# Kernel tuning notes

Hardware: AMD Instinct MI355X
Metric: run time of the kernel (lower is better)

Reference implementation:

```python
import jax, jax.numpy as jnp
import numpy as np

DIM = 1024
NUM_HEADS = 16
HEAD_DIM = DIM // NUM_HEADS
ROPE_BASE = 10000.0


def _rope_cache(seq_len, head_dim, dtype=jnp.float32):
    inv_freq = 1.0 / (ROPE_BASE ** (jnp.arange(0, head_dim, 2, dtype=jnp.float32) / head_dim))
    t = jnp.arange(seq_len, dtype=jnp.float32)
    freqs = jnp.einsum('i,j->ij', t, inv_freq)          # [S, hd/2]
    emb = jnp.concatenate([freqs, freqs], axis=-1)       # [S, hd]
    return jnp.cos(emb).astype(dtype), jnp.sin(emb).astype(dtype)


def _rotate_half(x):
    x1, x2 = jnp.split(x, 2, axis=-1)
    return jnp.concatenate([-x2, x1], axis=-1)


def setup_inputs() -> dict:
    key = jax.random.key(0)
    k1, k2, k3 = jax.random.split(key, 3)
    B, S, D = 2, 2048, DIM
    x = jax.random.normal(k1, (B, S, D), dtype=jnp.float32)
    mask = jnp.tril(jnp.ones((S, S), dtype=jnp.bool_))   # causal mask
    w_qkv = jax.random.normal(k2, (D, 3 * D), dtype=jnp.float32) * (D ** -0.5)
    w_out = jax.random.normal(k3, (D, D), dtype=jnp.float32) * (D ** -0.5)
    return {"x": x, "w_qkv": w_qkv, "w_out": w_out, "mask": mask}


def reference(x, w_qkv, w_out, mask):
    B, S, D = x.shape
    H, hd = NUM_HEADS, HEAD_DIM
    qkv = x @ w_qkv                                       # [B,S,3D]
    q, k, v = jnp.split(qkv, 3, axis=-1)
    # [B,H,S,hd]
    q = q.reshape(B, S, H, hd).transpose(0, 2, 1, 3)
    k = k.reshape(B, S, H, hd).transpose(0, 2, 1, 3)
    v = v.reshape(B, S, H, hd).transpose(0, 2, 1, 3)
    cos, sin = _rope_cache(S, hd, q.dtype)               # [S,hd]
    q = q * cos + _rotate_half(q) * sin
    k = k * cos + _rotate_half(k) * sin
    scale = hd ** -0.5
    scores = jnp.einsum('bhqd,bhkd->bhqk', q, k) * scale  # [B,H,S,S]
    neg = jnp.finfo(scores.dtype).min
    scores = jnp.where(mask[None, None, :, :], scores, neg)
    attn = jax.nn.softmax(scores, axis=-1)                # dropout off (eval)
    out = jnp.einsum('bhqk,bhkd->bhqd', attn, v)
    out = out.transpose(0, 2, 1, 3).reshape(B, S, D)
    return out @ w_out
```

## Files before the change

### kernel.cpp

```cpp
#include <hip/hip_runtime.h>

typedef __attribute__((ext_vector_type(8))) short short8;
typedef __attribute__((ext_vector_type(4))) float f32x4;
typedef __attribute__((ext_vector_type(16))) float f32x16;

__device__ __forceinline__ unsigned short f2bf(float f) {
    unsigned u = __builtin_bit_cast(unsigned, f);
    u += 0x7FFFu + ((u >> 16) & 1u);
    return (unsigned short)(u >> 16);
}
__device__ __forceinline__ short8 ld_frag(const uint4* p, size_t idx16) {
    return __builtin_bit_cast(short8, p[idx16]);
}
__device__ __forceinline__ unsigned cvt_pk_bf16(float lo, float hi) {
    unsigned r;
    asm("v_cvt_pk_bf16_f32 %0, %1, %2" : "=v"(r) : "v"(lo), "v"(hi));
    return r;
}
__device__ __forceinline__ void gload_lds16(const void* g, void* l) {
    __builtin_amdgcn_global_load_lds((const __attribute__((address_space(1))) void*)g,
                                     (__attribute__((address_space(3))) void*)l, 16, 0, 0);
}

__global__ __launch_bounds__(256) void prep_kernel(const float* __restrict__ x, unsigned short* __restrict__ xb,
                                                   const float* __restrict__ wqkv, unsigned short* __restrict__ wqkvT,
                                                   const float* __restrict__ wout, unsigned short* __restrict__ woutT,
                                                   float* __restrict__ cosT, float* __restrict__ sinT) {
    __shared__ float t[32][33];
    int bid = blockIdx.x, tid = threadIdx.x;
    if (bid < 256) {
        int idx = bid * 256 + tid;
        int s = idx >> 5, i = idx & 31;
        float inv = powf(10000.f, -(float)i / 32.f);
        float ang = (float)s * inv;
        cosT[idx] = cosf(ang);
        sinT[idx] = sinf(ang);
        return;
    }
    if (bid < 4352) {
        int i = (bid - 256) * 256 + tid;
        float4 v = reinterpret_cast<const float4*>(x)[i];
        ushort4 o;
        o.x = f2bf(v.x); o.y = f2bf(v.y); o.z = f2bf(v.z); o.w = f2bf(v.w);
        reinterpret_cast<ushort4*>(xb)[i] = o;
        return;
    }
    const float* in; unsigned short* out; int R, C, c0, r0;
    if (bid < 7424) {
        int b2 = bid - 4352;
        in = wqkv; out = wqkvT; R = 1024; C = 3072;
        c0 = (b2 % 96) * 32; r0 = (b2 / 96) * 32;
    } else {
        int b2 = bid - 7424;
        in = wout; out = woutT; R = 1024; C = 1024;
        c0 = (b2 % 32) * 32; r0 = (b2 / 32) * 32;
    }
    int tx = tid & 31, ty = tid >> 5;
    for (int i = 0; i < 4; ++i)
        t[ty + i * 8][tx] = in[(size_t)(r0 + ty + i * 8) * C + c0 + tx];
    __syncthreads();
    for (int i = 0; i < 4; ++i)
        out[(size_t)(c0 + ty + i * 8) * R + r0 + tx] = f2bf(t[tx][ty + i * 8]);
}

template <bool OUT_BF16, int NF>
__global__ __launch_bounds__(256) void gemm_bt_kernel(const unsigned short* __restrict__ A,
                                                      const unsigned short* __restrict__ Bt,
                                                      void* __restrict__ Cout,
                                                      int M, int N, int K) {
    constexpr int BN = NF * 32;
    __shared__ __align__(16) unsigned short As[2][128 * 32];
    __shared__ __align__(16) unsigned short Bs[2][BN * 32];
    int tid = threadIdx.x;
    int lane = tid & 63;
    int w = tid >> 6;
    int wm = w >> 1, wn = w & 1;
    int m0 = blockIdx.y * 128, n0 = blockIdx.x * BN;
    int rq = lane >> 4, cl = lane & 15;

    f32x4 acc[4][NF] = {};
    const uint4* As4 = reinterpret_cast<const uint4*>(As);
    const uint4* Bs4 = reinterpret_cast<const uint4*>(Bs);

    #pragma unroll
    for (int i = 0; i < 2; ++i) {
        int c = i * 256 + tid;
        int r = c >> 2, cc = c & 3;
        gload_lds16(A + (size_t)(m0 + r) * K + cc * 8,
                    (char*)As[0] + (size_t)(i * 256 + w * 64) * 16);
    }
    #pragma unroll
    for (int i = 0; i < NF / 2; ++i) {
        int c = i * 256 + tid;
        int r = c >> 2, cc = c & 3;
        gload_lds16(Bt + (size_t)(n0 + r) * K + cc * 8,
                    (char*)Bs[0] + (size_t)(i * 256 + w * 64) * 16);
    }
    __syncthreads();
    int cur = 0;

    for (int k0 = 0; k0 < K; k0 += 32) {
        short8 af[4], bfr[NF];
        #pragma unroll
        for (int mf = 0; mf < 4; ++mf) {
            int row = wm * 64 + mf * 16 + cl;
            af[mf] = ld_frag(As4, cur * 512 + row * 4 + rq);
        }
        #pragma unroll
        for (int nf = 0; nf < NF; ++nf) {
            int row = wn * (NF * 16) + nf * 16 + cl;
            bfr[nf] = ld_frag(Bs4, cur * (NF * 128) + row * 4 + rq);
        }
        if (k0 + 32 < K) {
            int kn = k0 + 32;
            #pragma unroll
            for (int i = 0; i < 2; ++i) {
                int c = i * 256 + tid;
                int r = c >> 2, cc = c & 3;
                gload_lds16(A + (size_t)(m0 + r) * K + kn + cc * 8,
                            (char*)As[cur ^ 1] + (size_t)(i * 256 + w * 64) * 16);
            }
            #pragma unroll
            for (int i = 0; i < NF / 2; ++i) {
                int c = i * 256 + tid;
                int r = c >> 2, cc = c & 3;
                gload_lds16(Bt + (size_t)(n0 + r) * K + kn + cc * 8,
                            (char*)Bs[cur ^ 1] + (size_t)(i * 256 + w * 64) * 16);
            }
        }
        __builtin_amdgcn_s_setprio(1);
        #pragma unroll
        for (int mf = 0; mf < 4; ++mf)
            #pragma unroll
            for (int nf = 0; nf < NF; ++nf)
                acc[mf][nf] = __builtin_amdgcn_mfma_f32_16x16x32_bf16(af[mf], bfr[nf], acc[mf][nf], 0, 0, 0);
        __builtin_amdgcn_s_setprio(0);
        __syncthreads();
        cur ^= 1;
    }
    #pragma unroll
    for (int mf = 0; mf < 4; ++mf)
        #pragma unroll
        for (int nf = 0; nf < NF; ++nf)
            #pragma unroll
            for (int r = 0; r < 4; ++r) {
                size_t row = m0 + wm * 64 + mf * 16 + rq * 4 + r;
                size_t col = n0 + wn * (NF * 16) + nf * 16 + cl;
                float v = acc[mf][nf][r];
                if (OUT_BF16)
                    ((unsigned short*)Cout)[row * N + col] = f2bf(v);
                else
                    ((float*)Cout)[row * N + col] = v;
            }
}

__global__ __launch_bounds__(256) void gemm_qkv_rope_kernel(const unsigned short* __restrict__ A,
                                                            const unsigned short* __restrict__ Bt,
                                                            const float* __restrict__ cosT,
                                                            const float* __restrict__ sinT,
                                                            unsigned short* __restrict__ Qb,
                                                            unsigned short* __restrict__ Kb,
                                                            unsigned short* __restrict__ VT) {
    const int K = 1024;
    __shared__ __align__(16) unsigned short As[2][128 * 32];
    __shared__ __align__(16) unsigned short Bs[2][128 * 32];
    int tid = threadIdx.x;
    int lane = tid & 63;
    int w = tid >> 6;
    int wm = w >> 1, wn = w & 1;
    int m0 = blockIdx.y * 128, n0 = blockIdx.x * 128;
    int rq = lane >> 4, cl = lane & 15;

    f32x4 acc[4][4] = {};
    const uint4* As4 = reinterpret_cast<const uint4*>(As);
    const uint4* Bs4 = reinterpret_cast<const uint4*>(Bs);

    #pragma unroll
    for (int i = 0; i < 2; ++i) {
        int c = i * 256 + tid;
        int r = c >> 2, cc = c & 3;
        gload_lds16(A + (size_t)(m0 + r) * K + cc * 8,
                    (char*)As[0] + (size_t)(i * 256 + w * 64) * 16);
        gload_lds16(Bt + (size_t)(n0 + r) * K + cc * 8,
                    (char*)Bs[0] + (size_t)(i * 256 + w * 64) * 16);
    }
    __syncthreads();
    int cur = 0;

    for (int k0 = 0; k0 < K; k0 += 32) {
        short8 af[4], bfr[4];
        #pragma unroll
        for (int mf = 0; mf < 4; ++mf)
            af[mf] = ld_frag(As4, cur * 512 + (wm * 64 + mf * 16 + cl) * 4 + rq);
        #pragma unroll
        for (int nf = 0; nf < 4; ++nf)
            bfr[nf] = ld_frag(Bs4, cur * 512 + (wn * 64 + nf * 16 + cl) * 4 + rq);
        if (k0 + 32 < K) {
            int kn = k0 + 32;
            #pragma unroll
            for (int i = 0; i < 2; ++i) {
                int c = i * 256 + tid;
                int r = c >> 2, cc = c & 3;
                gload_lds16(A + (size_t)(m0 + r) * K + kn + cc * 8,
                            (char*)As[cur ^ 1] + (size_t)(i * 256 + w * 64) * 16);
                gload_lds16(Bt + (size_t)(n0 + r) * K + kn + cc * 8,
                            (char*)Bs[cur ^ 1] + (size_t)(i * 256 + w * 64) * 16);
            }
        }
        __builtin_amdgcn_s_setprio(1);
        #pragma unroll
        for (int mf = 0; mf < 4; ++mf)
            #pragma unroll
            for (int nf = 0; nf < 4; ++nf)
                acc[mf][nf] = __builtin_amdgcn_mfma_f32_16x16x32_bf16(af[mf], bfr[nf], acc[mf][nf], 0, 0, 0);
        __builtin_amdgcn_s_setprio(0);
        __syncthreads();
        cur ^= 1;
    }

    const float QSCALE = 0.125f * 1.44269504088896f;
    int colbase = n0 + wn * 64;
    int sect = colbase >> 10;
    int h = (colbase >> 6) & 15;
    #pragma unroll
    for (int mf = 0; mf < 4; ++mf) {
        int row0 = m0 + wm * 64 + mf * 16 + rq * 4;
        int b = row0 >> 11;
        int s0r = row0 & 2047;
        size_t ho = (size_t)(b * 16 + h);
        if (sect == 2) {
            #pragma unroll
            for (int nf = 0; nf < 4; ++nf) {
                int d = nf * 16 + cl;
                ushort4 o;
                o.x = f2bf(acc[mf][nf][0]);
                o.y = f2bf(acc[mf][nf][1]);
                o.z = f2bf(acc[mf][nf][2]);
                o.w = f2bf(acc[mf][nf][3]);
                *reinterpret_cast<ushort4*>(VT + (ho * 64 + d) * 2048 + s0r) = o;
            }
        } else {
            unsigned short* dst = (sect == 0) ? Qb : Kb;
            float scale = (sect == 0) ? QSCALE : 1.0f;
            #pragma unroll
            for (int nf = 0; nf < 4; ++nf) {
                int d = nf * 16 + cl;
                int f = ((nf & 1) << 4) + cl;
                #pragma unroll
                for (int r = 0; r < 4; ++r) {
                    int s = s0r + r;
                    float cs = cosT[s * 32 + f], sn = sinT[s * 32 + f];
                    float val = acc[mf][nf][r], pair = acc[mf][nf ^ 2][r];
                    float out = (nf < 2) ? val * cs - pair * sn : val * cs + pair * sn;
                    dst[(ho * 2048 + s) * 64 + d] = f2bf(out * scale);
                }
            }
        }
    }
}

__global__ __launch_bounds__(256) void flash_attn_kernel(const unsigned short* __restrict__ Qb,
                                                         const unsigned short* __restrict__ Kb,
                                                         const unsigned short* __restrict__ VT,
                                                         unsigned short* __restrict__ Oattn) {
    const int S = 2048;
    __shared__ __align__(16) char smem[4 * 8192 + 512];
    char* KsB = smem;
    char* VsB = smem + 2 * 8192;
    int tid = threadIdx.x, lane = tid & 63, w = tid >> 6;
    int qsub = w & 1, kvh = w >> 1;
    int gid = blockIdx.x;
    int hh = gid & 31;
    int cp = gid >> 5;
    size_t headOff = (size_t)hh * S * 64;
    const unsigned short* Kg = Kb + headOff;
    const unsigned short* Vg = VT + headOff;
    const uint4* Qg4 = reinterpret_cast<const uint4*>(Qb + headOff);
    int l31 = lane & 31, hi = lane >> 5;

    int sr[2], sj[2];
    #pragma unroll
    for (int i = 0; i < 2; ++i) {
        int cch = i * 256 + tid;
        sr[i] = cch >> 3;
        sj[i] = ((cch & 7) ^ (sr[i] & 7)) * 8;
    }
    float* mo = reinterpret_cast<float*>(smem);
    float* ml = reinterpret_cast<float*>(smem + 16384);

    #pragma unroll
    for (int ph = 0; ph < 2; ++ph) {
        int c = ph ? (31 - cp) : cp;
        int q0 = c * 64;
        int qw = q0 + qsub * 32;
        int qrow = qw + l31;

        short8 qf[4];
        #pragma unroll
        for (int cc = 0; cc < 4; ++cc)
            qf[cc] = ld_frag(Qg4, (size_t)qrow * 8 + cc * 2 + hi);

        f32x16 oacc0 = {}, oacc1 = {};
        float l = 0.f;
        int nk = c + 1;

        #pragma unroll
        for (int i = 0; i < 2; ++i) {
            gload_lds16(Kg + sr[i] * 64 + sj[i], KsB + (i * 256 + w * 64) * 16);
            gload_lds16(Vg + (size_t)sr[i] * S + sj[i], VsB + (i * 256 + w * 64) * 16);
        }
        __syncthreads();
        int cur = 0;

        for (int kt = 0; kt < nk; ++kt) {
            int kv0 = kt * 64;
            int kvbase = kv0 + kvh * 32;
            bool active = kvbase <= qw + 31;
            short8 ka[4], va[4];
            if (active) {
                const char* Kt = KsB + cur * 8192;
                const char* Vt = VsB + cur * 8192;
                int r = kvh * 32 + l31;
                #pragma unroll
                for (int cc = 0; cc < 4; ++cc)
                    ka[cc] = __builtin_bit_cast(short8, *reinterpret_cast<const uint4*>(
                        Kt + r * 128 + (((2 * cc + hi) ^ (r & 7)) * 16)));
                #pragma unroll
                for (int t = 0; t < 2; ++t) {
                    va[t] = __builtin_bit_cast(short8, *reinterpret_cast<const uint4*>(
                        Vt + l31 * 128 + (((kvh * 4 + 2 * t + hi) ^ (l31 & 7)) * 16)));
                    va[2 + t] = __builtin_bit_cast(short8, *reinterpret_cast<const uint4*>(
                        Vt + (32 + l31) * 128 + (((kvh * 4 + 2 * t + hi) ^ ((32 + l31) & 7)) * 16)));
                }
            }
            if (kt + 1 < nk) {
                int kn = kv0 + 64;
                #pragma unroll
                for (int i = 0; i < 2; ++i) {
                    gload_lds16(Kg + (kn + sr[i]) * 64 + sj[i],
                                KsB + (cur ^ 1) * 8192 + (i * 256 + w * 64) * 16);
                    gload_lds16(Vg + (size_t)sr[i] * S + kn + sj[i],
                                VsB + (cur ^ 1) * 8192 + (i * 256 + w * 64) * 16);
                }
            }
            if (active) {
                f32x16 s = {};
                __builtin_amdgcn_s_setprio(1);
                #pragma unroll
                for (int cc = 0; cc < 4; ++cc)
                    s = __builtin_amdgcn_mfma_f32_32x32x16_bf16(ka[cc], qf[cc], s, 0, 0, 0);
                __builtin_amdgcn_s_setprio(0);

                if (kvbase + 31 > qw) {
                    #pragma unroll
                    for (int r = 0; r < 16; ++r) {
                        int kva = kvbase + (r & 3) + 8 * (r >> 2) + 4 * hi;
                        s[r] = (kva <= qrow) ? s[r] : -1e30f;
                    }
                }
                #pragma unroll
                for (int r = 0; r < 16; ++r) s[r] = exp2f(s[r]);
                float rp0 = ((s[0] + s[4]) + (s[8] + s[12])) + ((s[1] + s[5]) + (s[9] + s[13]));
                float rp1 = ((s[2] + s[6]) + (s[10] + s[14])) + ((s[3] + s[7]) + (s[11] + s[15]));
                float rs = rp0 + rp1;
                rs += __shfl_xor(rs, 32);
                l += rs;

                unsigned wd[8];
                #pragma unroll
                for (int i = 0; i < 8; ++i) wd[i] = cvt_pk_bf16(s[2 * i], s[2 * i + 1]);
                unsigned e0 = (unsigned)__shfl_xor((int)(hi ? wd[0] : wd[2]), 32);
                unsigned e1 = (unsigned)__shfl_xor((int)(hi ? wd[1] : wd[3]), 32);
                unsigned e2 = (unsigned)__shfl_xor((int)(hi ? wd[4] : wd[6]), 32);
                unsigned e3 = (unsigned)__shfl_xor((int)(hi ? wd[5] : wd[7]), 32);
                uint4 p0 = hi ? uint4{e0, e1, wd[2], wd[3]} : uint4{wd[0], wd[1], e0, e1};
                uint4 p1 = hi ? uint4{e2, e3, wd[6], wd[7]} : uint4{wd[4], wd[5], e2, e3};
                short8 pb0 = __builtin_bit_cast(short8, p0);
                short8 pb1 = __builtin_bit_cast(short8, p1);

                __builtin_amdgcn_s_setprio(1);
                oacc0 = __builtin_amdgcn_mfma_f32_32x32x16_bf16(va[0], pb0, oacc0, 0, 0, 0);
                oacc0 = __builtin_amdgcn_mfma_f32_32x32x16_bf16(va[1], pb1, oacc0, 0, 0, 0);
                oacc1 = __builtin_amdgcn_mfma_f32_32x32x16_bf16(va[2], pb0, oacc1, 0, 0, 0);
                oacc1 = __builtin_amdgcn_mfma_f32_32x32x16_bf16(va[3], pb1, oacc1, 0, 0, 0);
                __builtin_amdgcn_s_setprio(0);
            }
            __syncthreads();
            cur ^= 1;
        }

        if (kvh) {
            #pragma unroll
            for (int r = 0; r < 16; ++r) {
                mo[(r * 2 + qsub) * 64 + lane]        = oacc0[r];
                mo[((16 + r) * 2 + qsub) * 64 + lane] = oacc1[r];
            }
            ml[qsub * 64 + lane] = l;
        }
        __syncthreads();
        if (!kvh) {
            l += ml[qsub * 64 + lane];
            float invl = 1.f / l;
            size_t orow = ((size_t)((hh >> 4) * 2048 + qrow)) * 1024 + (hh & 15) * 64;
            #pragma unroll
            for (int du = 0; du < 2; ++du) {
                const f32x16& oa = du ? oacc1 : oacc0;
                #pragma unroll
                for (int gq = 0; gq < 4; ++gq) {
                    ushort4 o;
                    #pragma unroll
                    for (int e = 0; e < 4; ++e) {
                        int r = 4 * gq + e;
                        float v = (oa[r] + mo[((du * 16 + r) * 2 + qsub) * 64 + lane]) * invl;
                        ((unsigned short*)&o)[e] = f2bf(v);
                    }
                    int d = du * 32 + 4 * hi + 8 * gq;
                    *reinterpret_cast<ushort4*>(Oattn + orow + d) = o;
                }
            }
        }
        __syncthreads();
    }
}

extern "C" void kernel_launch(void* const* d_in, const int* in_sizes, int n_in,
                              void* d_out, int out_size, void* d_ws, size_t ws_size,
                              hipStream_t stream) {
    const float* x    = (const float*)d_in[0];
    const float* wqkv = (const float*)d_in[1];
    const float* wout = (const float*)d_in[2];

    char* ws = (char*)d_ws;
    unsigned short* xb    = (unsigned short*)(ws);
    unsigned short* wqkvT = (unsigned short*)(ws + (8ull  << 20));
    unsigned short* woutT = (unsigned short*)(ws + (14ull << 20));
    unsigned short* Qb    = (unsigned short*)(ws + (40ull << 20));
    unsigned short* Kb    = (unsigned short*)(ws + (48ull << 20));
    unsigned short* VT    = (unsigned short*)(ws + (56ull << 20));
    unsigned short* Oat   = (unsigned short*)(ws + (64ull << 20));
    float* cosT           = (float*)(ws + (72ull << 20));
    float* sinT           = (float*)(ws + (72ull << 20) + (256u << 10));

    prep_kernel<<<8448, 256, 0, stream>>>(x, xb, wqkv, wqkvT, wout, woutT, cosT, sinT);
    gemm_qkv_rope_kernel<<<dim3(24, 32), 256, 0, stream>>>(xb, wqkvT, cosT, sinT, Qb, Kb, VT);
    flash_attn_kernel<<<512, 256, 0, stream>>>(Qb, Kb, VT, Oat);
    gemm_bt_kernel<false, 2><<<dim3(16, 32), 256, 0, stream>>>(Oat, woutT, d_out, 4096, 1024, 1024);
}
```

Baseline: 113.5 us.

## Triple-buffer LDS staging with explicit vmcnt waits in GEMMs and attention

Moves the two GEMM kernels and the attention kernel from double-buffered LDS staging to a three-stage ring. Prefetch now runs two tiles ahead, and each iteration waits with a partial s_waitcnt vmcnt and one barrier instead of a full __syncthreads at the end. The aim is to hide more global-load latency and cut the barrier cost per K step. In exchange it uses more LDS per block, which may lower occupancy, and it depends on the hand-tuned vmcnt counts matching the number of loads each thread issues.

```diff
diff --git a/kernel.cpp b/kernel.cpp
--- a/kernel.cpp
+++ b/kernel.cpp
@@ -21,6 +21,9 @@
     __builtin_amdgcn_global_load_lds((const __attribute__((address_space(1))) void*)g,
                                      (__attribute__((address_space(3))) void*)l, 16, 0, 0);
 }
+__device__ __forceinline__ void wait_vm4() { asm volatile("s_waitcnt vmcnt(4)" ::: "memory"); __builtin_amdgcn_sched_barrier(0); }
+__device__ __forceinline__ void wait_vm3() { asm volatile("s_waitcnt vmcnt(3)" ::: "memory"); __builtin_amdgcn_sched_barrier(0); }
+__device__ __forceinline__ void wait_vm0() { asm volatile("s_waitcnt vmcnt(0)" ::: "memory"); __builtin_amdgcn_sched_barrier(0); }
 
 __global__ __launch_bounds__(256) void prep_kernel(const float* __restrict__ x, unsigned short* __restrict__ xb,
                                                    const float* __restrict__ wqkv, unsigned short* __restrict__ wqkvT,
@@ -69,8 +72,8 @@
                                                       void* __restrict__ Cout,
                                                       int M, int N, int K) {
     constexpr int BN = NF * 32;
-    __shared__ __align__(16) unsigned short As[2][128 * 32];
-    __shared__ __align__(16) unsigned short Bs[2][BN * 32];
+    __shared__ __align__(16) unsigned short As[3][128 * 32];
+    __shared__ __align__(16) unsigned short Bs[3][BN * 32];
     int tid = threadIdx.x;
     int lane = tid & 63;
     int w = tid >> 6;
@@ -82,51 +85,44 @@
     const uint4* As4 = reinterpret_cast<const uint4*>(As);
     const uint4* Bs4 = reinterpret_cast<const uint4*>(Bs);
 
-    #pragma unroll
-    for (int i = 0; i < 2; ++i) {
-        int c = i * 256 + tid;
-        int r = c >> 2, cc = c & 3;
-        gload_lds16(A + (size_t)(m0 + r) * K + cc * 8,
-                    (char*)As[0] + (size_t)(i * 256 + w * 64) * 16);
-    }
-    #pragma unroll
-    for (int i = 0; i < NF / 2; ++i) {
-        int c = i * 256 + tid;
-        int r = c >> 2, cc = c & 3;
-        gload_lds16(Bt + (size_t)(n0 + r) * K + cc * 8,
-                    (char*)Bs[0] + (size_t)(i * 256 + w * 64) * 16);
-    }
-    __syncthreads();
-    int cur = 0;
-
-    for (int k0 = 0; k0 < K; k0 += 32) {
+    auto stage = [&](int k0, int buf) {
+        #pragma unroll
+        for (int i = 0; i < 2; ++i) {
+            int c = i * 256 + tid;
+            int r = c >> 2, cc = c & 3;
+            gload_lds16(A + (size_t)(m0 + r) * K + k0 + cc * 8,
+                        (char*)As[buf] + (size_t)(i * 256 + w * 64) * 16);
+        }
+        #pragma unroll
+        for (int i = 0; i < NF / 2; ++i) {
+            int c = i * 256 + tid;
+            int r = c >> 2, cc = c & 3;
+            gload_lds16(Bt + (size_t)(n0 + r) * K + k0 + cc * 8,
+                        (char*)Bs[buf] + (size_t)(i * 256 + w * 64) * 16);
+        }
+    };
+
+    int nk = K / 32;
+    stage(0, 0);
+    if (nk > 1) stage(32, 1);
+    int b0 = 0, b2 = 2;
+
+    for (int it = 0; it < nk; ++it) {
+        if (it + 1 < nk) { if constexpr (NF == 2) wait_vm3(); else wait_vm4(); }
+        else             wait_vm0();
+        __builtin_amdgcn_s_barrier();
+        if (it + 2 < nk) stage((it + 2) * 32, b2);
+
         short8 af[4], bfr[NF];
         #pragma unroll
         for (int mf = 0; mf < 4; ++mf) {
             int row = wm * 64 + mf * 16 + cl;
-            af[mf] = ld_frag(As4, cur * 512 + row * 4 + rq);
+            af[mf] = ld_frag(As4, b0 * 512 + row * 4 + rq);
         }
         #pragma unroll
         for (int nf = 0; nf < NF; ++nf) {
             int row = wn * (NF * 16) + nf * 16 + cl;
-            bfr[nf] = ld_frag(Bs4, cur * (NF * 128) + row * 4 + rq);
-        }
-        if (k0 + 32 < K) {
-            int kn = k0 + 32;
-            #pragma unroll
-            for (int i = 0; i < 2; ++i) {
-                int c = i * 256 + tid;
-                int r = c >> 2, cc = c & 3;
-                gload_lds16(A + (size_t)(m0 + r) * K + kn + cc * 8,
-                            (char*)As[cur ^ 1] + (size_t)(i * 256 + w * 64) * 16);
-            }
-            #pragma unroll
-            for (int i = 0; i < NF / 2; ++i) {
-                int c = i * 256 + tid;
-                int r = c >> 2, cc = c & 3;
-                gload_lds16(Bt + (size_t)(n0 + r) * K + kn + cc * 8,
-                            (char*)Bs[cur ^ 1] + (size_t)(i * 256 + w * 64) * 16);
-            }
+            bfr[nf] = ld_frag(Bs4, b0 * (NF * 128) + row * 4 + rq);
         }
         __builtin_amdgcn_s_setprio(1);
         #pragma unroll
@@ -135,8 +131,8 @@
             for (int nf = 0; nf < NF; ++nf)
                 acc[mf][nf] = __builtin_amdgcn_mfma_f32_16x16x32_bf16(af[mf], bfr[nf], acc[mf][nf], 0, 0, 0);
         __builtin_amdgcn_s_setprio(0);
-        __syncthreads();
-        cur ^= 1;
+        b0 = (b0 == 2) ? 0 : b0 + 1;
+        b2 = (b2 == 2) ? 0 : b2 + 1;
     }
     #pragma unroll
     for (int mf = 0; mf < 4; ++mf)
@@ -162,8 +158,8 @@
                                                             unsigned short* __restrict__ Kb,
                                                             unsigned short* __restrict__ VT) {
     const int K = 1024;
-    __shared__ __align__(16) unsigned short As[2][128 * 32];
-    __shared__ __align__(16) unsigned short Bs[2][128 * 32];
+    __shared__ __align__(16) unsigned short As[3][128 * 32];
+    __shared__ __align__(16) unsigned short Bs[3][128 * 32];
     int tid = threadIdx.x;
     int lane = tid & 63;
     int w = tid >> 6;
@@ -175,38 +171,35 @@
     const uint4* As4 = reinterpret_cast<const uint4*>(As);
     const uint4* Bs4 = reinterpret_cast<const uint4*>(Bs);
 
-    #pragma unroll
-    for (int i = 0; i < 2; ++i) {
-        int c = i * 256 + tid;
-        int r = c >> 2, cc = c & 3;
-        gload_lds16(A + (size_t)(m0 + r) * K + cc * 8,
-                    (char*)As[0] + (size_t)(i * 256 + w * 64) * 16);
-        gload_lds16(Bt + (size_t)(n0 + r) * K + cc * 8,
-                    (char*)Bs[0] + (size_t)(i * 256 + w * 64) * 16);
-    }
-    __syncthreads();
-    int cur = 0;
-
-    for (int k0 = 0; k0 < K; k0 += 32) {
+    auto stage = [&](int k0, int buf) {
+        #pragma unroll
+        for (int i = 0; i < 2; ++i) {
+            int c = i * 256 + tid;
+            int r = c >> 2, cc = c & 3;
+            gload_lds16(A + (size_t)(m0 + r) * K + k0 + cc * 8,
+                        (char*)As[buf] + (size_t)(i * 256 + w * 64) * 16);
+            gload_lds16(Bt + (size_t)(n0 + r) * K + k0 + cc * 8,
+                        (char*)Bs[buf] + (size_t)(i * 256 + w * 64) * 16);
+        }
+    };
+
+    stage(0, 0);
+    stage(32, 1);
+    int b0 = 0, b2 = 2;
+
+    for (int it = 0; it < 32; ++it) {
+        if (it + 1 < 32) wait_vm4();
+        else             wait_vm0();
+        __builtin_amdgcn_s_barrier();
+        if (it + 2 < 32) stage((it + 2) * 32, b2);
+
         short8 af[4], bfr[4];
         #pragma unroll
         for (int mf = 0; mf < 4; ++mf)
-            af[mf] = ld_frag(As4, cur * 512 + (wm * 64 + mf * 16 + cl) * 4 + rq);
+            af[mf] = ld_frag(As4, b0 * 512 + (wm * 64 + mf * 16 + cl) * 4 + rq);
         #pragma unroll
         for (int nf = 0; nf < 4; ++nf)
-            bfr[nf] = ld_frag(Bs4, cur * 512 + (wn * 64 + nf * 16 + cl) * 4 + rq);
-        if (k0 + 32 < K) {
-            int kn = k0 + 32;
-            #pragma unroll
-            for (int i = 0; i < 2; ++i) {
-                int c = i * 256 + tid;
-                int r = c >> 2, cc = c & 3;
-                gload_lds16(A + (size_t)(m0 + r) * K + kn + cc * 8,
-                            (char*)As[cur ^ 1] + (size_t)(i * 256 + w * 64) * 16);
-                gload_lds16(Bt + (size_t)(n0 + r) * K + kn + cc * 8,
-                            (char*)Bs[cur ^ 1] + (size_t)(i * 256 + w * 64) * 16);
-            }
-        }
+            bfr[nf] = ld_frag(Bs4, b0 * 512 + (wn * 64 + nf * 16 + cl) * 4 + rq);
         __builtin_amdgcn_s_setprio(1);
         #pragma unroll
         for (int mf = 0; mf < 4; ++mf)
@@ -214,8 +207,8 @@
             for (int nf = 0; nf < 4; ++nf)
                 acc[mf][nf] = __builtin_amdgcn_mfma_f32_16x16x32_bf16(af[mf], bfr[nf], acc[mf][nf], 0, 0, 0);
         __builtin_amdgcn_s_setprio(0);
-        __syncthreads();
-        cur ^= 1;
+        b0 = (b0 == 2) ? 0 : b0 + 1;
+        b2 = (b2 == 2) ? 0 : b2 + 1;
     }
 
     const float QSCALE = 0.125f * 1.44269504088896f;
@@ -264,9 +257,7 @@
                                                          const unsigned short* __restrict__ VT,
                                                          unsigned short* __restrict__ Oattn) {
     const int S = 2048;
-    __shared__ __align__(16) char smem[4 * 8192 + 512];
-    char* KsB = smem;
-    char* VsB = smem + 2 * 8192;
+    __shared__ __align__(16) char smem[3 * 16384 + 512];
     int tid = threadIdx.x, lane = tid & 63, w = tid >> 6;
     int qsub = w & 1, kvh = w >> 1;
     int gid = blockIdx.x;
@@ -286,7 +277,17 @@
         sj[i] = ((cch & 7) ^ (sr[i] & 7)) * 8;
     }
     float* mo = reinterpret_cast<float*>(smem);
-    float* ml = reinterpret_cast<float*>(smem + 16384);
+    float* ml = reinterpret_cast<float*>(smem + 3 * 16384);
+
+    auto stage = [&](int kt, int b) {
+        char* base = smem + b * 16384;
+        int kn = kt * 64;
+        #pragma unroll
+        for (int i = 0; i < 2; ++i) {
+            gload_lds16(Kg + (size_t)(kn + sr[i]) * 64 + sj[i], base + (i * 256 + w * 64) * 16);
+            gload_lds16(Vg + (size_t)sr[i] * S + kn + sj[i], base + 8192 + (i * 256 + w * 64) * 16);
+        }
+    };
 
     #pragma unroll
     for (int ph = 0; ph < 2; ++ph) {
@@ -304,22 +305,21 @@
         float l = 0.f;
         int nk = c + 1;
 
-        #pragma unroll
-        for (int i = 0; i < 2; ++i) {
-            gload_lds16(Kg + sr[i] * 64 + sj[i], KsB + (i * 256 + w * 64) * 16);
-            gload_lds16(Vg + (size_t)sr[i] * S + sj[i], VsB + (i * 256 + w * 64) * 16);
-        }
-        __syncthreads();
-        int cur = 0;
+        stage(0, 0);
+        if (nk > 1) stage(1, 1);
+        int b0 = 0, b2 = 2;
 
         for (int kt = 0; kt < nk; ++kt) {
-            int kv0 = kt * 64;
-            int kvbase = kv0 + kvh * 32;
-            bool active = kvbase <= qw + 31;
-            short8 ka[4], va[4];
-            if (active) {
-                const char* Kt = KsB + cur * 8192;
-                const char* Vt = VsB + cur * 8192;
+            if (kt + 1 < nk) wait_vm4();
+            else             wait_vm0();
+            __builtin_amdgcn_s_barrier();
+            if (kt + 2 < nk) stage(kt + 2, b2);
+
+            int kvbase = kt * 64 + kvh * 32;
+            if (kvbase <= qw + 31) {
+                const char* Kt = smem + b0 * 16384;
+                const char* Vt = Kt + 8192;
+                short8 ka[4], va[4];
                 int r = kvh * 32 + l31;
                 #pragma unroll
                 for (int cc = 0; cc < 4; ++cc)
@@ -332,18 +332,7 @@
                     va[2 + t] = __builtin_bit_cast(short8, *reinterpret_cast<const uint4*>(
                         Vt + (32 + l31) * 128 + (((kvh * 4 + 2 * t + hi) ^ ((32 + l31) & 7)) * 16)));
                 }
-            }
-            if (kt + 1 < nk) {
-                int kn = kv0 + 64;
-                #pragma unroll
-                for (int i = 0; i < 2; ++i) {
-                    gload_lds16(Kg + (kn + sr[i]) * 64 + sj[i],
-                                KsB + (cur ^ 1) * 8192 + (i * 256 + w * 64) * 16);
-                    gload_lds16(Vg + (size_t)sr[i] * S + kn + sj[i],
-                                VsB + (cur ^ 1) * 8192 + (i * 256 + w * 64) * 16);
-                }
-            }
-            if (active) {
+
                 f32x16 s = {};
                 __builtin_amdgcn_s_setprio(1);
                 #pragma unroll
@@ -353,13 +342,13 @@
 
                 if (kvbase + 31 > qw) {
                     #pragma unroll
-                    for (int r = 0; r < 16; ++r) {
-                        int kva = kvbase + (r & 3) + 8 * (r >> 2) + 4 * hi;
-                        s[r] = (kva <= qrow) ? s[r] : -1e30f;
+                    for (int r2 = 0; r2 < 16; ++r2) {
+                        int kva = kvbase + (r2 & 3) + 8 * (r2 >> 2) + 4 * hi;
+                        s[r2] = (kva <= qrow) ? s[r2] : -1e30f;
                     }
                 }
                 #pragma unroll
-                for (int r = 0; r < 16; ++r) s[r] = exp2f(s[r]);
+                for (int r2 = 0; r2 < 16; ++r2) s[r2] = exp2f(s[r2]);
                 float rp0 = ((s[0] + s[4]) + (s[8] + s[12])) + ((s[1] + s[5]) + (s[9] + s[13]));
                 float rp1 = ((s[2] + s[6]) + (s[10] + s[14])) + ((s[3] + s[7]) + (s[11] + s[15]));
                 float rs = rp0 + rp1;
@@ -385,9 +374,11 @@
                 oacc1 = __builtin_amdgcn_mfma_f32_32x32x16_bf16(va[3], pb1, oacc1, 0, 0, 0);
                 __builtin_amdgcn_s_setprio(0);
             }
-            __syncthreads();
-            cur ^= 1;
-        }
+            b0 = (b0 == 2) ? 0 : b0 + 1;
+            b2 = (b2 == 2) ? 0 : b2 + 1;
+        }
+
+        __syncthreads();
 
         if (kvh) {
             #pragma unroll
```

After: 118.1 us. 1.04x slower.

## Process both paired causal query chunks concurrently in one KV sweep

Applied to the files above, without the earlier changes.

The flash attention kernel used to handle its two paired query chunks (cp and 31-cp) one after the other, streaming the K/V tiles twice. Now wave pairs split the two chunks and each wave covers 64 query rows against its 32-key slice. All chunks share a single sweep of 32-cp K/V tiles, so each tile is loaded once for both chunks and the per-phase prologue and syncs go away. The cost is doubled accumulator registers (four f32x16), which may reduce occupancy, and waves on the short chunk idle for most rounds.

```diff
diff --git a/kernel.cpp b/kernel.cpp
--- a/kernel.cpp
+++ b/kernel.cpp
@@ -264,11 +264,9 @@
                                                          const unsigned short* __restrict__ VT,
                                                          unsigned short* __restrict__ Oattn) {
     const int S = 2048;
-    __shared__ __align__(16) char smem[4 * 8192 + 512];
-    char* KsB = smem;
-    char* VsB = smem + 2 * 8192;
+    __shared__ __align__(16) char smem[2 * 16384 + 1024];
     int tid = threadIdx.x, lane = tid & 63, w = tid >> 6;
-    int qsub = w & 1, kvh = w >> 1;
+    int half = w & 1, kvh = w >> 1;
     int gid = blockIdx.x;
     int hh = gid & 31;
     int cp = gid >> 5;
@@ -278,6 +276,11 @@
     const uint4* Qg4 = reinterpret_cast<const uint4*>(Qb + headOff);
     int l31 = lane & 31, hi = lane >> 5;
 
+    int c = half ? (31 - cp) : cp;
+    int q0 = c * 64;
+    int nk = c + 1;
+    int rounds = 32 - cp;
+
     int sr[2], sj[2];
     #pragma unroll
     for (int i = 0; i < 2; ++i) {
@@ -285,86 +288,78 @@
         sr[i] = cch >> 3;
         sj[i] = ((cch & 7) ^ (sr[i] & 7)) * 8;
     }
-    float* mo = reinterpret_cast<float*>(smem);
-    float* ml = reinterpret_cast<float*>(smem + 16384);
-
-    #pragma unroll
-    for (int ph = 0; ph < 2; ++ph) {
-        int c = ph ? (31 - cp) : cp;
-        int q0 = c * 64;
-        int qw = q0 + qsub * 32;
-        int qrow = qw + l31;
-
-        short8 qf[4];
+
+    short8 qf[2][4];
+    #pragma unroll
+    for (int qh = 0; qh < 2; ++qh)
         #pragma unroll
         for (int cc = 0; cc < 4; ++cc)
-            qf[cc] = ld_frag(Qg4, (size_t)qrow * 8 + cc * 2 + hi);
-
-        f32x16 oacc0 = {}, oacc1 = {};
-        float l = 0.f;
-        int nk = c + 1;
-
+            qf[qh][cc] = ld_frag(Qg4, (size_t)(q0 + qh * 32 + l31) * 8 + cc * 2 + hi);
+
+    f32x16 oacc00 = {}, oacc01 = {}, oacc10 = {}, oacc11 = {};
+    float l0 = 0.f, l1 = 0.f;
+
+    auto stage = [&](int kt, int b) {
+        char* base = smem + b * 16384;
+        int kn = kt * 64;
         #pragma unroll
         for (int i = 0; i < 2; ++i) {
-            gload_lds16(Kg + sr[i] * 64 + sj[i], KsB + (i * 256 + w * 64) * 16);
-            gload_lds16(Vg + (size_t)sr[i] * S + sj[i], VsB + (i * 256 + w * 64) * 16);
-        }
-        __syncthreads();
-        int cur = 0;
-
-        for (int kt = 0; kt < nk; ++kt) {
-            int kv0 = kt * 64;
-            int kvbase = kv0 + kvh * 32;
-            bool active = kvbase <= qw + 31;
-            short8 ka[4], va[4];
-            if (active) {
-                const char* Kt = KsB + cur * 8192;
-                const char* Vt = VsB + cur * 8192;
-                int r = kvh * 32 + l31;
-                #pragma unroll
-                for (int cc = 0; cc < 4; ++cc)
-                    ka[cc] = __builtin_bit_cast(short8, *reinterpret_cast<const uint4*>(
-                        Kt + r * 128 + (((2 * cc + hi) ^ (r & 7)) * 16)));
-                #pragma unroll
-                for (int t = 0; t < 2; ++t) {
-                    va[t] = __builtin_bit_cast(short8, *reinterpret_cast<const uint4*>(
-                        Vt + l31 * 128 + (((kvh * 4 + 2 * t + hi) ^ (l31 & 7)) * 16)));
-                    va[2 + t] = __builtin_bit_cast(short8, *reinterpret_cast<const uint4*>(
-                        Vt + (32 + l31) * 128 + (((kvh * 4 + 2 * t + hi) ^ ((32 + l31) & 7)) * 16)));
-                }
-            }
-            if (kt + 1 < nk) {
-                int kn = kv0 + 64;
-                #pragma unroll
-                for (int i = 0; i < 2; ++i) {
-                    gload_lds16(Kg + (kn + sr[i]) * 64 + sj[i],
-                                KsB + (cur ^ 1) * 8192 + (i * 256 + w * 64) * 16);
-                    gload_lds16(Vg + (size_t)sr[i] * S + kn + sj[i],
-                                VsB + (cur ^ 1) * 8192 + (i * 256 + w * 64) * 16);
-                }
-            }
-            if (active) {
+            gload_lds16(Kg + (size_t)(kn + sr[i]) * 64 + sj[i], base + (i * 256 + w * 64) * 16);
+            gload_lds16(Vg + (size_t)sr[i] * S + kn + sj[i], base + 8192 + (i * 256 + w * 64) * 16);
+        }
+    };
+
+    stage(0, 0);
+    __syncthreads();
+    int cur = 0;
+
+    for (int kt = 0; kt < rounds; ++kt) {
+        bool active = kt < nk;
+        int kvbase = kt * 64 + kvh * 32;
+        short8 ka[4], va[4];
+        if (active) {
+            const char* Kt = smem + cur * 16384;
+            const char* Vt = Kt + 8192;
+            int r = kvh * 32 + l31;
+            #pragma unroll
+            for (int cc = 0; cc < 4; ++cc)
+                ka[cc] = __builtin_bit_cast(short8, *reinterpret_cast<const uint4*>(
+                    Kt + r * 128 + (((2 * cc + hi) ^ (r & 7)) * 16)));
+            #pragma unroll
+            for (int t = 0; t < 2; ++t) {
+                va[t] = __builtin_bit_cast(short8, *reinterpret_cast<const uint4*>(
+                    Vt + l31 * 128 + (((kvh * 4 + 2 * t + hi) ^ (l31 & 7)) * 16)));
+                va[2 + t] = __builtin_bit_cast(short8, *reinterpret_cast<const uint4*>(
+                    Vt + (32 + l31) * 128 + (((kvh * 4 + 2 * t + hi) ^ ((32 + l31) & 7)) * 16)));
+            }
+        }
+        if (kt + 1 < rounds) stage(kt + 1, cur ^ 1);
+        if (active) {
+            #pragma unroll
+            for (int qh = 0; qh < 2; ++qh) {
+                int qwq = q0 + qh * 32;
+                int qrow = qwq + l31;
                 f32x16 s = {};
                 __builtin_amdgcn_s_setprio(1);
                 #pragma unroll
                 for (int cc = 0; cc < 4; ++cc)
-                    s = __builtin_amdgcn_mfma_f32_32x32x16_bf16(ka[cc], qf[cc], s, 0, 0, 0);
+                    s = __builtin_amdgcn_mfma_f32_32x32x16_bf16(ka[cc], qh ? qf[1][cc] : qf[0][cc], s, 0, 0, 0);
                 __builtin_amdgcn_s_setprio(0);
 
-                if (kvbase + 31 > qw) {
+                if (kvbase + 31 > qwq) {
                     #pragma unroll
-                    for (int r = 0; r < 16; ++r) {
-                        int kva = kvbase + (r & 3) + 8 * (r >> 2) + 4 * hi;
-                        s[r] = (kva <= qrow) ? s[r] : -1e30f;
+                    for (int r2 = 0; r2 < 16; ++r2) {
+                        int kva = kvbase + (r2 & 3) + 8 * (r2 >> 2) + 4 * hi;
+                        s[r2] = (kva <= qrow) ? s[r2] : -1e30f;
                     }
                 }
                 #pragma unroll
-                for (int r = 0; r < 16; ++r) s[r] = exp2f(s[r]);
+                for (int r2 = 0; r2 < 16; ++r2) s[r2] = exp2f(s[r2]);
                 float rp0 = ((s[0] + s[4]) + (s[8] + s[12])) + ((s[1] + s[5]) + (s[9] + s[13]));
                 float rp1 = ((s[2] + s[6]) + (s[10] + s[14])) + ((s[3] + s[7]) + (s[11] + s[15]));
                 float rs = rp0 + rp1;
                 rs += __shfl_xor(rs, 32);
-                l += rs;
+                if (qh) l1 += rs; else l0 += rs;
 
                 unsigned wd[8];
                 #pragma unroll
@@ -379,39 +374,55 @@
                 short8 pb1 = __builtin_bit_cast(short8, p1);
 
                 __builtin_amdgcn_s_setprio(1);
-                oacc0 = __builtin_amdgcn_mfma_f32_32x32x16_bf16(va[0], pb0, oacc0, 0, 0, 0);
-                oacc0 = __builtin_amdgcn_mfma_f32_32x32x16_bf16(va[1], pb1, oacc0, 0, 0, 0);
-                oacc1 = __builtin_amdgcn_mfma_f32_32x32x16_bf16(va[2], pb0, oacc1, 0, 0, 0);
-                oacc1 = __builtin_amdgcn_mfma_f32_32x32x16_bf16(va[3], pb1, oacc1, 0, 0, 0);
+                if (qh) {
+                    oacc10 = __builtin_amdgcn_mfma_f32_32x32x16_bf16(va[0], pb0, oacc10, 0, 0, 0);
+                    oacc10 = __builtin_amdgcn_mfma_f32_32x32x16_bf16(va[1], pb1, oacc10, 0, 0, 0);
+                    oacc11 = __builtin_amdgcn_mfma_f32_32x32x16_bf16(va[2], pb0, oacc11, 0, 0, 0);
+                    oacc11 = __builtin_amdgcn_mfma_f32_32x32x16_bf16(va[3], pb1, oacc11, 0, 0, 0);
+                } else {
+                    oacc00 = __builtin_amdgcn_mfma_f32_32x32x16_bf16(va[0], pb0, oacc00, 0, 0, 0);
+                    oacc00 = __builtin_amdgcn_mfma_f32_32x32x16_bf16(va[1], pb1, oacc00, 0, 0, 0);
+                    oacc01 = __builtin_amdgcn_mfma_f32_32x32x16_bf16(va[2], pb0, oacc01, 0, 0, 0);
+                    oacc01 = __builtin_amdgcn_mfma_f32_32x32x16_bf16(va[3], pb1, oacc01, 0, 0, 0);
+                }
                 __builtin_amdgcn_s_setprio(0);
             }
-            __syncthreads();
-            cur ^= 1;
-        }
-
-        if (kvh) {
-            #pragma unroll
-            for (int r = 0; r < 16; ++r) {
-                mo[(r * 2 + qsub) * 64 + lane]        = oacc0[r];
-                mo[((16 + r) * 2 + qsub) * 64 + lane] = oacc1[r];
-            }
-            ml[qsub * 64 + lane] = l;
         }
         __syncthreads();
-        if (!kvh) {
-            l += ml[qsub * 64 + lane];
+        cur ^= 1;
+    }
+
+    float* mo = reinterpret_cast<float*>(smem);
+    float* ml = reinterpret_cast<float*>(smem + 32768);
+    if (kvh) {
+        #pragma unroll
+        for (int r = 0; r < 16; ++r) {
+            mo[((half * 2 + 0) * 32 + r) * 64 + lane]      = oacc00[r];
+            mo[((half * 2 + 0) * 32 + 16 + r) * 64 + lane] = oacc01[r];
+            mo[((half * 2 + 1) * 32 + r) * 64 + lane]      = oacc10[r];
+            mo[((half * 2 + 1) * 32 + 16 + r) * 64 + lane] = oacc11[r];
+        }
+        ml[(half * 2 + 0) * 64 + lane] = l0;
+        ml[(half * 2 + 1) * 64 + lane] = l1;
+    }
+    __syncthreads();
+    if (!kvh) {
+        #pragma unroll
+        for (int qh = 0; qh < 2; ++qh) {
+            float l = (qh ? l1 : l0) + ml[(half * 2 + qh) * 64 + lane];
             float invl = 1.f / l;
+            int qrow = q0 + qh * 32 + l31;
             size_t orow = ((size_t)((hh >> 4) * 2048 + qrow)) * 1024 + (hh & 15) * 64;
             #pragma unroll
             for (int du = 0; du < 2; ++du) {
-                const f32x16& oa = du ? oacc1 : oacc0;
+                const f32x16& oa = qh ? (du ? oacc11 : oacc10) : (du ? oacc01 : oacc00);
                 #pragma unroll
                 for (int gq = 0; gq < 4; ++gq) {
                     ushort4 o;
                     #pragma unroll
                     for (int e = 0; e < 4; ++e) {
                         int r = 4 * gq + e;
-                        float v = (oa[r] + mo[((du * 16 + r) * 2 + qsub) * 64 + lane]) * invl;
+                        float v = (oa[r] + mo[((half * 2 + qh) * 32 + du * 16 + r) * 64 + lane]) * invl;
                         ((unsigned short*)&o)[e] = f2bf(v);
                     }
                     int d = du * 32 + 4 * hi + 8 * gq;
@@ -419,7 +430,6 @@
                 }
             }
         }
-        __syncthreads();
     }
 }
 
```

Measured after the change: 156.2 us. 37.6% more time.

## Stage two KV tiles per round to halve barrier count in flash attention

Applied to the files above, without the earlier changes.

The flash attention loop now loads two 64-row K/V tiles per pipeline stage into a larger double-buffered shared memory region (64KB). It processes both tiles before a single __syncthreads, so the main loop takes half as many barriers and prefetches twice as much data ahead. In exchange the block uses more LDS, which may lower occupancy, and the prefetch of round rd+1 is issued after the first sub-tile's fragment loads.

```diff
diff --git a/kernel.cpp b/kernel.cpp
--- a/kernel.cpp
+++ b/kernel.cpp
@@ -264,9 +264,7 @@
                                                          const unsigned short* __restrict__ VT,
                                                          unsigned short* __restrict__ Oattn) {
     const int S = 2048;
-    __shared__ __align__(16) char smem[4 * 8192 + 512];
-    char* KsB = smem;
-    char* VsB = smem + 2 * 8192;
+    __shared__ __align__(16) char smem[2 * 32768 + 512];
     int tid = threadIdx.x, lane = tid & 63, w = tid >> 6;
     int qsub = w & 1, kvh = w >> 1;
     int gid = blockIdx.x;
@@ -303,87 +301,100 @@
         f32x16 oacc0 = {}, oacc1 = {};
         float l = 0.f;
         int nk = c + 1;
-
-        #pragma unroll
-        for (int i = 0; i < 2; ++i) {
-            gload_lds16(Kg + sr[i] * 64 + sj[i], KsB + (i * 256 + w * 64) * 16);
-            gload_lds16(Vg + (size_t)sr[i] * S + sj[i], VsB + (i * 256 + w * 64) * 16);
-        }
+        int nr = (nk + 1) >> 1;
+
+        auto stage2 = [&](int rd, int b) {
+            char* base = smem + b * 32768;
+            #pragma unroll
+            for (int sub = 0; sub < 2; ++sub) {
+                int kt = 2 * rd + sub;
+                if (kt < nk) {
+                    int kn = kt * 64;
+                    #pragma unroll
+                    for (int i = 0; i < 2; ++i) {
+                        gload_lds16(Kg + (size_t)(kn + sr[i]) * 64 + sj[i],
+                                    base + sub * 8192 + (i * 256 + w * 64) * 16);
+                        gload_lds16(Vg + (size_t)sr[i] * S + kn + sj[i],
+                                    base + 16384 + sub * 8192 + (i * 256 + w * 64) * 16);
+                    }
+                }
+            }
+        };
+
+        stage2(0, 0);
         __syncthreads();
         int cur = 0;
 
-        for (int kt = 0; kt < nk; ++kt) {
-            int kv0 = kt * 64;
-            int kvbase = kv0 + kvh * 32;
-            bool active = kvbase <= qw + 31;
-            short8 ka[4], va[4];
-            if (active) {
-                const char* Kt = KsB + cur * 8192;
-                const char* Vt = VsB + cur * 8192;
-                int r = kvh * 32 + l31;
-                #pragma unroll
-                for (int cc = 0; cc < 4; ++cc)
-                    ka[cc] = __builtin_bit_cast(short8, *reinterpret_cast<const uint4*>(
-                        Kt + r * 128 + (((2 * cc + hi) ^ (r & 7)) * 16)));
-                #pragma unroll
-                for (int t = 0; t < 2; ++t) {
-                    va[t] = __builtin_bit_cast(short8, *reinterpret_cast<const uint4*>(
-                        Vt + l31 * 128 + (((kvh * 4 + 2 * t + hi) ^ (l31 & 7)) * 16)));
-                    va[2 + t] = __builtin_bit_cast(short8, *reinterpret_cast<const uint4*>(
-                        Vt + (32 + l31) * 128 + (((kvh * 4 + 2 * t + hi) ^ ((32 + l31) & 7)) * 16)));
-                }
-            }
-            if (kt + 1 < nk) {
-                int kn = kv0 + 64;
-                #pragma unroll
-                for (int i = 0; i < 2; ++i) {
-                    gload_lds16(Kg + (kn + sr[i]) * 64 + sj[i],
-                                KsB + (cur ^ 1) * 8192 + (i * 256 + w * 64) * 16);
-                    gload_lds16(Vg + (size_t)sr[i] * S + kn + sj[i],
-                                VsB + (cur ^ 1) * 8192 + (i * 256 + w * 64) * 16);
-                }
-            }
-            if (active) {
-                f32x16 s = {};
-                __builtin_amdgcn_s_setprio(1);
-                #pragma unroll
-                for (int cc = 0; cc < 4; ++cc)
-                    s = __builtin_amdgcn_mfma_f32_32x32x16_bf16(ka[cc], qf[cc], s, 0, 0, 0);
-                __builtin_amdgcn_s_setprio(0);
-
-                if (kvbase + 31 > qw) {
-                    #pragma unroll
-                    for (int r = 0; r < 16; ++r) {
-                        int kva = kvbase + (r & 3) + 8 * (r >> 2) + 4 * hi;
-                        s[r] = (kva <= qrow) ? s[r] : -1e30f;
+        for (int rd = 0; rd < nr; ++rd) {
+            bool staged = false;
+            #pragma unroll
+            for (int sub = 0; sub < 2; ++sub) {
+                int kt = 2 * rd + sub;
+                int kvbase = kt * 64 + kvh * 32;
+                bool active = (kt < nk) && (kvbase <= qw + 31);
+                short8 ka[4], va[4];
+                if (active) {
+                    const char* Kt = smem + cur * 32768 + sub * 8192;
+                    const char* Vt = smem + cur * 32768 + 16384 + sub * 8192;
+                    int r = kvh * 32 + l31;
+                    #pragma unroll
+                    for (int cc = 0; cc < 4; ++cc)
+                        ka[cc] = __builtin_bit_cast(short8, *reinterpret_cast<const uint4*>(
+                            Kt + r * 128 + (((2 * cc + hi) ^ (r & 7)) * 16)));
+                    #pragma unroll
+                    for (int t = 0; t < 2; ++t) {
+                        va[t] = __builtin_bit_cast(short8, *reinterpret_cast<const uint4*>(
+                            Vt + l31 * 128 + (((kvh * 4 + 2 * t + hi) ^ (l31 & 7)) * 16)));
+                        va[2 + t] = __builtin_bit_cast(short8, *reinterpret_cast<const uint4*>(
+                            Vt + (32 + l31) * 128 + (((kvh * 4 + 2 * t + hi) ^ ((32 + l31) & 7)) * 16)));
                     }
                 }
-                #pragma unroll
-                for (int r = 0; r < 16; ++r) s[r] = exp2f(s[r]);
-                float rp0 = ((s[0] + s[4]) + (s[8] + s[12])) + ((s[1] + s[5]) + (s[9] + s[13]));
-                float rp1 = ((s[2] + s[6]) + (s[10] + s[14])) + ((s[3] + s[7]) + (s[11] + s[15]));
-                float rs = rp0 + rp1;
-                rs += __shfl_xor(rs, 32);
-                l += rs;
-
-                unsigned wd[8];
-                #pragma unroll
-                for (int i = 0; i < 8; ++i) wd[i] = cvt_pk_bf16(s[2 * i], s[2 * i + 1]);
-                unsigned e0 = (unsigned)__shfl_xor((int)(hi ? wd[0] : wd[2]), 32);
-                unsigned e1 = (unsigned)__shfl_xor((int)(hi ? wd[1] : wd[3]), 32);
-                unsigned e2 = (unsigned)__shfl_xor((int)(hi ? wd[4] : wd[6]), 32);
-                unsigned e3 = (unsigned)__shfl_xor((int)(hi ? wd[5] : wd[7]), 32);
-                uint4 p0 = hi ? uint4{e0, e1, wd[2], wd[3]} : uint4{wd[0], wd[1], e0, e1};
-                uint4 p1 = hi ? uint4{e2, e3, wd[6], wd[7]} : uint4{wd[4], wd[5], e2, e3};
-                short8 pb0 = __builtin_bit_cast(short8, p0);
-                short8 pb1 = __builtin_bit_cast(short8, p1);
-
-                __builtin_amdgcn_s_setprio(1);
-                oacc0 = __builtin_amdgcn_mfma_f32_32x32x16_bf16(va[0], pb0, oacc0, 0, 0, 0);
-                oacc0 = __builtin_amdgcn_mfma_f32_32x32x16_bf16(va[1], pb1, oacc0, 0, 0, 0);
-                oacc1 = __builtin_amdgcn_mfma_f32_32x32x16_bf16(va[2], pb0, oacc1, 0, 0, 0);
-                oacc1 = __builtin_amdgcn_mfma_f32_32x32x16_bf16(va[3], pb1, oacc1, 0, 0, 0);
-                __builtin_amdgcn_s_setprio(0);
+                if (!staged) {
+                    if (rd + 1 < nr) stage2(rd + 1, cur ^ 1);
+                    staged = true;
+                }
+                if (active) {
+                    f32x16 s = {};
+                    __builtin_amdgcn_s_setprio(1);
+                    #pragma unroll
+                    for (int cc = 0; cc < 4; ++cc)
+                        s = __builtin_amdgcn_mfma_f32_32x32x16_bf16(ka[cc], qf[cc], s, 0, 0, 0);
+                    __builtin_amdgcn_s_setprio(0);
+
+                    if (kvbase + 31 > qw) {
+                        #pragma unroll
+                        for (int r = 0; r < 16; ++r) {
+                            int kva = kvbase + (r & 3) + 8 * (r >> 2) + 4 * hi;
+                            s[r] = (kva <= qrow) ? s[r] : -1e30f;
+                        }
+                    }
+                    #pragma unroll
+                    for (int r = 0; r < 16; ++r) s[r] = exp2f(s[r]);
+                    float rp0 = ((s[0] + s[4]) + (s[8] + s[12])) + ((s[1] + s[5]) + (s[9] + s[13]));
+                    float rp1 = ((s[2] + s[6]) + (s[10] + s[14])) + ((s[3] + s[7]) + (s[11] + s[15]));
+                    float rs = rp0 + rp1;
+                    rs += __shfl_xor(rs, 32);
+                    l += rs;
+
+                    unsigned wd[8];
+                    #pragma unroll
+                    for (int i = 0; i < 8; ++i) wd[i] = cvt_pk_bf16(s[2 * i], s[2 * i + 1]);
+                    unsigned e0 = (unsigned)__shfl_xor((int)(hi ? wd[0] : wd[2]), 32);
+                    unsigned e1 = (unsigned)__shfl_xor((int)(hi ? wd[1] : wd[3]), 32);
+                    unsigned e2 = (unsigned)__shfl_xor((int)(hi ? wd[4] : wd[6]), 32);
+                    unsigned e3 = (unsigned)__shfl_xor((int)(hi ? wd[5] : wd[7]), 32);
+                    uint4 p0 = hi ? uint4{e0, e1, wd[2], wd[3]} : uint4{wd[0], wd[1], e0, e1};
+                    uint4 p1 = hi ? uint4{e2, e3, wd[6], wd[7]} : uint4{wd[4], wd[5], e2, e3};
+                    short8 pb0 = __builtin_bit_cast(short8, p0);
+                    short8 pb1 = __builtin_bit_cast(short8, p1);
+
+                    __builtin_amdgcn_s_setprio(1);
+                    oacc0 = __builtin_amdgcn_mfma_f32_32x32x16_bf16(va[0], pb0, oacc0, 0, 0, 0);
+                    oacc0 = __builtin_amdgcn_mfma_f32_32x32x16_bf16(va[1], pb1, oacc0, 0, 0, 0);
+                    oacc1 = __builtin_amdgcn_mfma_f32_32x32x16_bf16(va[2], pb0, oacc1, 0, 0, 0);
+                    oacc1 = __builtin_amdgcn_mfma_f32_32x32x16_bf16(va[3], pb1, oacc1, 0, 0, 0);
+                    __builtin_amdgcn_s_setprio(0);
+                }
             }
             __syncthreads();
             cur ^= 1;
```

Measured after the change: 110.0 us. -3.1%, faster.
